# Performance work log

Measured on AMD Instinct MI355X. Metric: run time of the kernel, lower is better.

The kernel has to match this reference:

```python
import jax, jax.numpy as jnp
import numpy as np

D_MODEL = 2048
NUM_Q_HEADS = 16
NUM_KV_HEADS = 4
HEAD_DIM = D_MODEL // NUM_Q_HEADS  # 128
NUM_GROUPS = NUM_Q_HEADS // NUM_KV_HEADS  # 4
ROPE_BASE = 10000.0


def _rope_cos_sin(seq_len, head_dim):
    inv_freq = 1.0 / (ROPE_BASE ** (jnp.arange(0, head_dim, 2, dtype=jnp.float32) / head_dim))
    t = jnp.arange(seq_len, dtype=jnp.float32)
    freqs = jnp.outer(t, inv_freq)            # [S, head_dim/2]
    emb = jnp.concatenate([freqs, freqs], -1)  # [S, head_dim]
    return jnp.cos(emb)[None, :, None, :], jnp.sin(emb)[None, :, None, :]


def _rotate_half(x):
    half = x.shape[-1] // 2
    return jnp.concatenate([-x[..., half:], x[..., :half]], axis=-1)


def setup_inputs() -> dict:
    key = jax.random.key(0)
    k0, k1, k2, k3, k4 = jax.random.split(key, 5)
    B, S = 2, 2048
    kv_dim = HEAD_DIM * NUM_KV_HEADS
    scale = D_MODEL ** -0.5
    return {
        "x": jax.random.normal(k0, (B, S, D_MODEL), jnp.float32),
        "attention_mask": jnp.ones((B, S), jnp.int32),
        "Wq": jax.random.normal(k1, (D_MODEL, D_MODEL), jnp.float32) * scale,
        "Wk": jax.random.normal(k2, (D_MODEL, kv_dim), jnp.float32) * scale,
        "Wv": jax.random.normal(k3, (D_MODEL, kv_dim), jnp.float32) * scale,
        "Wo": jax.random.normal(k4, (D_MODEL, D_MODEL), jnp.float32) * scale,
    }


def reference(x, attention_mask, Wq, Wk, Wv, Wo):
    B, S, _ = x.shape
    q = (x @ Wq).reshape(B, S, NUM_Q_HEADS, HEAD_DIM)
    k = (x @ Wk).reshape(B, S, NUM_KV_HEADS, HEAD_DIM)
    v = (x @ Wv).reshape(B, S, NUM_KV_HEADS, HEAD_DIM)

    cos, sin = _rope_cos_sin(S, HEAD_DIM)  # [1,S,1,hd]
    q = q * cos + _rotate_half(q) * sin
    k = k * cos + _rotate_half(k) * sin

    # [B, H, S, hd]; replicate KV heads across groups (repeat_interleave)
    q = q.transpose(0, 2, 1, 3)
    k = jnp.repeat(k.transpose(0, 2, 1, 3), NUM_GROUPS, axis=1)
    v = jnp.repeat(v.transpose(0, 2, 1, 3), NUM_GROUPS, axis=1)

    scale = HEAD_DIM ** -0.5
    scores = jnp.einsum("bhqd,bhkd->bhqk", q, k) * scale
    mask = attention_mask[:, None, None, :]  # [B,1,1,S] over keys
    scores = jnp.where(mask == 0, jnp.float32(-jnp.inf), scores)
    probs = jax.nn.softmax(scores, axis=-1)
    out = jnp.einsum("bhqk,bhkd->bhqd", probs, v)
    out = out.transpose(0, 2, 1, 3).reshape(B, S, D_MODEL)
    return out @ Wo
```

## Files before the change

kernel.cpp:

```cpp
#include <hip/hip_runtime.h>
#include <hip/hip_bf16.h>

typedef __attribute__((ext_vector_type(4))) float f32x4;
typedef __attribute__((ext_vector_type(16))) float f32x16;
typedef __attribute__((ext_vector_type(8))) short s16x8;
typedef __attribute__((ext_vector_type(4))) short s16x4;
typedef __attribute__((ext_vector_type(2))) unsigned int u32x2;

__device__ __forceinline__ float fexp2(float x) {
    float y; asm("v_exp_f32 %0, %1" : "=v"(y) : "v"(x)); return y;
}

__global__ void rope_tables(float* __restrict__ cosT, float* __restrict__ sinT) {
    const int s = blockIdx.x, j = threadIdx.x;
    const float inv = exp2f(-(float)j * (13.287712379549449f / 64.f));
    const float f = (float)s * inv;
    cosT[s * 64 + j] = cosf(f);
    sinT[s * 64 + j] = sinf(f);
}

__global__ void mask_bias(const int* __restrict__ mask, float* __restrict__ mb, int n) {
    const int i = blockIdx.x * 256 + threadIdx.x;
    if (i < n) mb[i] = (mask[i] == 0) ? -1e30f : 0.f;
}

__global__ __launch_bounds__(256)
void cast_f32_bf16(const float* __restrict__ src, __hip_bfloat16* __restrict__ dst, int n4) {
    const int i = blockIdx.x * 256 + threadIdx.x;
    if (i < n4) {
        f32x4 v = *reinterpret_cast<const f32x4*>(src + (size_t)i * 4);
        union { s16x4 v4; __hip_bfloat16 h[4]; } u;
#pragma unroll
        for (int j = 0; j < 4; ++j) u.h[j] = __float2bfloat16(v[j]);
        *reinterpret_cast<s16x4*>(dst + (size_t)i * 4) = u.v4;
    }
}

__global__ __launch_bounds__(256)
void transpose_cast_all(const float* __restrict__ Wq, const float* __restrict__ Wk,
                        const float* __restrict__ Wv, const float* __restrict__ Wo,
                        __hip_bfloat16* __restrict__ wqkv_t, __hip_bfloat16* __restrict__ wo_t) {
    __shared__ __align__(16) float t[32][33];
    const int tx = threadIdx.x, ty = threadIdx.y;
    const int xseg = blockIdx.x;
    const int r0 = blockIdx.y * 32;
    const float* src; __hip_bfloat16* dst; int C, c0;
    if (xseg < 64)      { src = Wq; dst = wqkv_t;                  C = 2048; c0 = xseg * 32; }
    else if (xseg < 80) { src = Wk; dst = wqkv_t + 2048ULL * 2048; C = 512;  c0 = (xseg - 64) * 32; }
    else if (xseg < 96) { src = Wv; dst = wqkv_t + 2560ULL * 2048; C = 512;  c0 = (xseg - 80) * 32; }
    else                { src = Wo; dst = wo_t;                    C = 2048; c0 = (xseg - 96) * 32; }
#pragma unroll
    for (int i = 0; i < 32; i += 8)
        t[ty + i][tx] = src[(size_t)(r0 + ty + i) * C + c0 + tx];
    __syncthreads();
#pragma unroll
    for (int i = 0; i < 32; i += 8)
        dst[(size_t)(c0 + ty + i) * 2048 + r0 + tx] = __float2bfloat16(t[tx][ty + i]);
}

__global__ __launch_bounds__(256)
void vt_transpose(const __hip_bfloat16* __restrict__ qkv, __hip_bfloat16* __restrict__ Vt) {
    __shared__ unsigned short t[32][33];
    const int tx = threadIdx.x, ty = threadIdx.y;
    const int s0 = blockIdx.x * 32, d0 = blockIdx.y * 32;
    const int bh = blockIdx.z, b = bh >> 2, hh = bh & 3;
    const unsigned short* q = (const unsigned short*)qkv;
#pragma unroll
    for (int i = 0; i < 32; i += 8)
        t[ty + i][tx] = q[(size_t)(b * 2048 + s0 + ty + i) * 3072 + 2560 + hh * 128 + d0 + tx];
    __syncthreads();
#pragma unroll
    for (int i = 0; i < 32; i += 8)
        ((unsigned short*)Vt)[((size_t)(bh * 128) + d0 + ty + i) * 2048 + s0 + tx] = t[tx][ty + i];
}

template<int NI, bool BF16OUT>
__global__ __launch_bounds__(512, 1)
void gemm256_bt(const __hip_bfloat16* __restrict__ A,
                const __hip_bfloat16* __restrict__ Bt,
                void* __restrict__ Cv, int M, int N, int K, int NX) {
    constexpr int NB = NI / 2;
    __shared__ __align__(16) __hip_bfloat16 sm[4][2][8192];
    const int tid = threadIdx.x;
    const int l = tid & 63, w = tid >> 6;
    const int lo = l & 15, hi = l >> 4;
    const int wm = w >> 2, wn = w & 3;
    const int id = blockIdx.x, slot = id >> 3;
    const int by = (id & 7) * 2 + slot / NX;
    const int bx = slot % NX;
    const int row0 = by * 256;
    const int col0 = bx * (NI * 64);
    const int nk = K >> 5;

    f32x4 acc[8][NI];
#pragma unroll
    for (int mi = 0; mi < 8; ++mi)
#pragma unroll
        for (int ni = 0; ni < NI; ++ni) acc[mi][ni] = f32x4{0.f, 0.f, 0.f, 0.f};

    auto stage = [&](int kt) {
        const int s = kt & 3, k0 = kt << 5;
#pragma unroll
        for (int i = 0; i < 2; ++i) {
            const int c = i * 512 + tid;
            const int r = c >> 2, sw = ((c & 3) ^ ((r >> 1) & 3)) * 8;
            __builtin_amdgcn_global_load_lds(
                (const __attribute__((address_space(1))) void*)(A + (size_t)(row0 + r) * K + k0 + sw),
                (__attribute__((address_space(3))) void*)(&sm[s][0][c * 8]), 16, 0, 0);
        }
#pragma unroll
        for (int i = 0; i < NB; ++i) {
            const int c = i * 512 + tid;
            const int r = c >> 2, sw = ((c & 3) ^ ((r >> 1) & 3)) * 8;
            __builtin_amdgcn_global_load_lds(
                (const __attribute__((address_space(1))) void*)(Bt + (size_t)(col0 + r) * K + k0 + sw),
                (__attribute__((address_space(3))) void*)(&sm[s][1][c * 8]), 16, 0, 0);
        }
    };

    stage(0); stage(1); stage(2);
    for (int kt = 0; kt < nk; ++kt) {
        const int s = kt & 3;
        if (kt < nk - 2) {
            if constexpr (NI == 4) asm volatile("s_waitcnt vmcnt(8)" ::: "memory");
            else                   asm volatile("s_waitcnt vmcnt(6)" ::: "memory");
        } else if (kt == nk - 2) {
            if constexpr (NI == 4) asm volatile("s_waitcnt vmcnt(4)" ::: "memory");
            else                   asm volatile("s_waitcnt vmcnt(3)" ::: "memory");
        } else {
            asm volatile("s_waitcnt vmcnt(0)" ::: "memory");
        }
        asm volatile("s_waitcnt lgkmcnt(0)" ::: "memory");
        asm volatile("s_barrier" ::: "memory");
        if (kt + 3 < nk) stage(kt + 3);

        s16x8 af[8], bf[NI];
        const int rsw = ((lo >> 1) & 3);
#pragma unroll
        for (int mi = 0; mi < 8; ++mi)
            af[mi] = *reinterpret_cast<const s16x8*>(
                &sm[s][0][(wm * 128 + mi * 16 + lo) * 32 + ((hi ^ rsw) * 8)]);
#pragma unroll
        for (int ni = 0; ni < NI; ++ni)
            bf[ni] = *reinterpret_cast<const s16x8*>(
                &sm[s][1][(wn * NI * 16 + ni * 16 + lo) * 32 + ((hi ^ rsw) * 8)]);
        __builtin_amdgcn_s_setprio(1);
#pragma unroll
        for (int mi = 0; mi < 8; ++mi)
#pragma unroll
            for (int ni = 0; ni < NI; ++ni)
                acc[mi][ni] = __builtin_amdgcn_mfma_f32_16x16x32_bf16(af[mi], bf[ni], acc[mi][ni], 0, 0, 0);
        __builtin_amdgcn_s_setprio(0);
    }
    const int rbase = row0 + wm * 128 + hi * 4;
    const int cbase = col0 + wn * NI * 16 + lo;
    if constexpr (BF16OUT) {
        __hip_bfloat16* C = (__hip_bfloat16*)Cv;
#pragma unroll
        for (int mi = 0; mi < 8; ++mi)
#pragma unroll
            for (int ni = 0; ni < NI; ++ni)
#pragma unroll
                for (int r = 0; r < 4; ++r)
                    C[(size_t)(rbase + mi * 16 + r) * N + cbase + ni * 16] =
                        __float2bfloat16(acc[mi][ni][r]);
    } else {
        float* C = (float*)Cv;
#pragma unroll
        for (int mi = 0; mi < 8; ++mi)
#pragma unroll
            for (int ni = 0; ni < NI; ++ni)
#pragma unroll
                for (int r = 0; r < 4; ++r)
                    C[(size_t)(rbase + mi * 16 + r) * N + cbase + ni * 16] = acc[mi][ni][r];
    }
}

__global__ __launch_bounds__(256)
void rope_scatter(const __hip_bfloat16* __restrict__ qkv,
                  const float* __restrict__ cosT, const float* __restrict__ sinT,
                  __hip_bfloat16* __restrict__ Qr, __hip_bfloat16* __restrict__ Kr) {
    const int m = blockIdx.y;
    const int col4 = blockIdx.x * 256 + threadIdx.x;
    if (col4 >= 640) return;
    const int col = col4 * 4;
    const int b = m >> 11, s = m & 2047;
    const int d = col & 127;
    const int j = d & 63;
    union { s16x4 v4; __hip_bfloat16 h[4]; } vv, pp, u;
    vv.v4 = *reinterpret_cast<const s16x4*>(qkv + (size_t)m * 3072 + col);
    pp.v4 = *reinterpret_cast<const s16x4*>(qkv + (size_t)m * 3072 + (col ^ 64));
    const f32x4 c4 = *reinterpret_cast<const f32x4*>(cosT + s * 64 + j);
    const f32x4 s4 = *reinterpret_cast<const f32x4*>(sinT + s * 64 + j);
    const float sgn = (d < 64) ? -1.f : 1.f;
#pragma unroll
    for (int i = 0; i < 4; ++i)
        u.h[i] = __float2bfloat16(__bfloat162float(vv.h[i]) * c4[i] +
                                  sgn * __bfloat162float(pp.h[i]) * s4[i]);
    if (col < 2048) {
        const int hh = col >> 7;
        *reinterpret_cast<s16x4*>(&Qr[((size_t)(b * 16 + hh) * 2048 + s) * 128 + d]) = u.v4;
    } else {
        const int hh = (col - 2048) >> 7;
        *reinterpret_cast<s16x4*>(&Kr[((size_t)(b * 4 + hh) * 2048 + s) * 128 + d]) = u.v4;
    }
}

__global__ __launch_bounds__(256, 2)
void attn_kernel(const __hip_bfloat16* __restrict__ Qr,
                 const __hip_bfloat16* __restrict__ Kr,
                 const __hip_bfloat16* __restrict__ Vt,
                 const float* __restrict__ maskb,
                 __hip_bfloat16* __restrict__ Oo) {
    const int S = 2048;
    const int id = blockIdx.x;
    const int v = (id & 7) * 64 + (id >> 3);
    const int qt = v & 15;
    const int bh = v >> 4;
    const int b = bh >> 4, h = bh & 15, kvh = h >> 2;
    const int tid = threadIdx.x;
    const int l = tid & 63, wv_ = tid >> 6;
    const int lq = l & 31, hi2 = l >> 5;
    __shared__ __align__(16) __hip_bfloat16 Ks[2][64 * 128];
    __shared__ __align__(16) __hip_bfloat16 Vs[2][128 * 64];

    const __hip_bfloat16* Qb = Qr + (size_t)(b * 16 + h) * S * 128;
    const __hip_bfloat16* Kb = Kr + (size_t)(b * 4 + kvh) * S * 128;
    const __hip_bfloat16* Vb = Vt + (size_t)(b * 4 + kvh) * 128 * S;
    const float* mrow = maskb + b * S;

    const int qrow = qt * 128 + wv_ * 32 + lq;
    s16x8 qf[8];
#pragma unroll
    for (int ks = 0; ks < 8; ++ks)
        qf[ks] = *reinterpret_cast<const s16x8*>(Qb + (size_t)qrow * 128 + ks * 16 + hi2 * 8);

    float m_run = 0.f, l_run = 0.f;
    f32x16 o[4];
#pragma unroll
    for (int dt = 0; dt < 4; ++dt)
#pragma unroll
        for (int r = 0; r < 16; ++r) o[dt][r] = 0.f;
    const float scale2 = 0.12751682f;

    const int krow = tid >> 4, kc8 = tid & 15;
    const int koff = (kc8 ^ (krow & 7)) * 8;
    const int vrow = tid >> 3, vc8 = tid & 7;
    const int voff = (vc8 ^ (vrow & 7)) * 8;

    s16x8 kreg[4], vreg[4];
    auto load_tile = [&](int kv0) {
#pragma unroll
        for (int i = 0; i < 4; ++i)
            kreg[i] = *reinterpret_cast<const s16x8*>(
                Kb + (size_t)(kv0 + i * 16 + krow) * 128 + kc8 * 8);
#pragma unroll
        for (int i = 0; i < 4; ++i)
            vreg[i] = *reinterpret_cast<const s16x8*>(
                Vb + (size_t)(i * 32 + vrow) * S + kv0 + vc8 * 8);
    };

    auto body = [&](int kt, __hip_bfloat16* Kc, __hip_bfloat16* Vc) {
        const int kv0 = kt * 64;
        f32x4 bi[2][4];
#pragma unroll
        for (int sub = 0; sub < 2; ++sub)
#pragma unroll
            for (int r4 = 0; r4 < 4; ++r4)
                bi[sub][r4] = *reinterpret_cast<const f32x4*>(
                    mrow + kv0 + sub * 32 + r4 * 8 + hi2 * 4);
#pragma unroll
        for (int i = 0; i < 4; ++i)
            *reinterpret_cast<s16x8*>(Kc + (i * 16 + krow) * 128 + koff) = kreg[i];
#pragma unroll
        for (int i = 0; i < 4; ++i)
            *reinterpret_cast<s16x8*>(Vc + (i * 32 + vrow) * 64 + voff) = vreg[i];
        if (kt < 31) load_tile(kv0 + 64);
        asm volatile("s_waitcnt lgkmcnt(0)" ::: "memory");
        asm volatile("s_barrier" ::: "memory");

        f32x16 sc[2];
#pragma unroll
        for (int sub = 0; sub < 2; ++sub)
#pragma unroll
            for (int r = 0; r < 16; ++r) sc[sub][r] = 0.f;
        __builtin_amdgcn_s_setprio(1);
#pragma unroll
        for (int sub = 0; sub < 2; ++sub) {
            const int kr = sub * 32 + lq;
            const int ksw = kr & 7;
#pragma unroll
            for (int ks = 0; ks < 8; ++ks) {
                s16x8 kf = *reinterpret_cast<const s16x8*>(
                    Kc + kr * 128 + (((ks * 2 + hi2) ^ ksw) * 8));
                sc[sub] = __builtin_amdgcn_mfma_f32_32x32x16_bf16(kf, qf[ks], sc[sub], 0, 0, 0);
            }
        }
        __builtin_amdgcn_s_setprio(0);
#pragma unroll
        for (int sub = 0; sub < 2; ++sub)
#pragma unroll
            for (int r = 0; r < 16; ++r)
                sc[sub][r] = fmaf(sc[sub][r], scale2, bi[sub][r >> 2][r & 3]);
        float mx = sc[0][0];
#pragma unroll
        for (int sub = 0; sub < 2; ++sub)
#pragma unroll
            for (int r = 0; r < 16; ++r) mx = fmaxf(mx, sc[sub][r]);
        float ss = 0.f;
#pragma unroll
        for (int sub = 0; sub < 2; ++sub)
#pragma unroll
            for (int r = 0; r < 16; ++r) {
                sc[sub][r] = fexp2(sc[sub][r] - m_run);
                ss += sc[sub][r];
            }
        mx = fmaxf(mx, __shfl_xor(mx, 32));
        if (__ballot(mx > m_run + 11.5417f) != 0ull) {
            const float mnew = fmaxf(m_run, mx);
            const float alpha = fexp2(m_run - mnew);
            m_run = mnew;
            l_run *= alpha;
            ss *= alpha;
#pragma unroll
            for (int sub = 0; sub < 2; ++sub)
#pragma unroll
                for (int r = 0; r < 16; ++r) sc[sub][r] *= alpha;
#pragma unroll
            for (int dt = 0; dt < 4; ++dt)
#pragma unroll
                for (int r = 0; r < 16; ++r) o[dt][r] *= alpha;
        }
        ss += __shfl_xor(ss, 32);
        l_run += ss;
        unsigned int wvp[8][2];
#pragma unroll
        for (int g = 0; g < 8; ++g) {
            const int sub = g >> 2, r4 = g & 3;
            asm("v_cvt_pk_bf16_f32 %0, %1, %2"
                : "=v"(wvp[g][0]) : "v"(sc[sub][r4 * 4 + 0]), "v"(sc[sub][r4 * 4 + 1]));
            asm("v_cvt_pk_bf16_f32 %0, %1, %2"
                : "=v"(wvp[g][1]) : "v"(sc[sub][r4 * 4 + 2]), "v"(sc[sub][r4 * 4 + 3]));
        }
        __builtin_amdgcn_s_setprio(1);
#pragma unroll
        for (int ks = 0; ks < 4; ++ks) {
            u32x2 r0 = __builtin_amdgcn_permlane32_swap(wvp[2 * ks][0], wvp[2 * ks + 1][0], false, false);
            u32x2 r1 = __builtin_amdgcn_permlane32_swap(wvp[2 * ks][1], wvp[2 * ks + 1][1], false, false);
            union { unsigned int u[4]; s16x8 v; } pf;
            pf.u[0] = r0.x; pf.u[1] = r1.x; pf.u[2] = r0.y; pf.u[3] = r1.y;
#pragma unroll
            for (int dt = 0; dt < 4; ++dt) {
                const int dvr = dt * 32 + lq;
                s16x8 vf = *reinterpret_cast<const s16x8*>(
                    Vc + dvr * 64 + (((ks * 2 + hi2) ^ (dvr & 7)) * 8));
                o[dt] = __builtin_amdgcn_mfma_f32_32x32x16_bf16(vf, pf.v, o[dt], 0, 0, 0);
            }
        }
        __builtin_amdgcn_s_setprio(0);
    };

    load_tile(0);
    for (int kt2 = 0; kt2 < 16; ++kt2) {
        body(2 * kt2,     &Ks[0][0], &Vs[0][0]);
        body(2 * kt2 + 1, &Ks[1][0], &Vs[1][0]);
    }
    const float inv = 1.f / l_run;
    const size_t obase = (size_t)(b * S + qt * 128 + wv_ * 32 + lq) * 2048 + h * 128;
#pragma unroll
    for (int dt = 0; dt < 4; ++dt)
#pragma unroll
        for (int r4 = 0; r4 < 4; ++r4) {
            union { s16x4 v4; __hip_bfloat16 hh[4]; } u;
#pragma unroll
            for (int j = 0; j < 4; ++j)
                u.hh[j] = __float2bfloat16(o[dt][r4 * 4 + j] * inv);
            *reinterpret_cast<s16x4*>(&Oo[obase + dt * 32 + r4 * 8 + hi2 * 4]) = u.v4;
        }
}

extern "C" void kernel_launch(void* const* d_in, const int* in_sizes, int n_in,
                              void* d_out, int out_size, void* d_ws, size_t ws_size,
                              hipStream_t stream) {
    const float* x  = (const float*)d_in[0];
    const int* mask = (const int*)d_in[1];
    const float* Wq = (const float*)d_in[2];
    const float* Wk = (const float*)d_in[3];
    const float* Wv = (const float*)d_in[4];
    const float* Wo = (const float*)d_in[5];
    float* out = (float*)d_out;

    char* ws = (char*)d_ws;
    size_t off = 0;
    auto alloc = [&](size_t bytes) -> void* {
        void* p = ws + off;
        off += (bytes + 255) & ~(size_t)255;
        return p;
    };
    __hip_bfloat16* xb     = (__hip_bfloat16*)alloc(4096ULL * 2048 * 2);
    __hip_bfloat16* wqkv_t = (__hip_bfloat16*)alloc(3072ULL * 2048 * 2);
    __hip_bfloat16* wo_t   = (__hip_bfloat16*)alloc(2048ULL * 2048 * 2);
    __hip_bfloat16* qkvb   = (__hip_bfloat16*)alloc(4096ULL * 3072 * 2);
    __hip_bfloat16* Kr     = (__hip_bfloat16*)alloc(2ULL * 4 * 2048 * 128 * 2);
    __hip_bfloat16* Vt     = (__hip_bfloat16*)alloc(2ULL * 4 * 2048 * 128 * 2);
    float*          cosT   = (float*)alloc(2048ULL * 64 * 4);
    float*          sinT   = (float*)alloc(2048ULL * 64 * 4);
    float*          maskb  = (float*)alloc(2ULL * 2048 * 4);
    __hip_bfloat16* attno  = (__hip_bfloat16*)alloc(4096ULL * 2048 * 2);
    __hip_bfloat16* Qr    = xb;

    rope_tables<<<dim3(2048), dim3(64), 0, stream>>>(cosT, sinT);
    mask_bias<<<dim3(16), dim3(256), 0, stream>>>(mask, maskb, 4096);
    cast_f32_bf16<<<dim3(8192), dim3(256), 0, stream>>>(x, xb, 2097152);
    transpose_cast_all<<<dim3(160, 64), dim3(32, 8), 0, stream>>>(Wq, Wk, Wv, Wo, wqkv_t, wo_t);

    gemm256_bt<4, true><<<dim3(192), dim3(512), 0, stream>>>(xb, wqkv_t, qkvb, 4096, 3072, 2048, 12);
    rope_scatter<<<dim3(3, 4096), dim3(256), 0, stream>>>(qkvb, cosT, sinT, Qr, Kr);
    vt_transpose<<<dim3(64, 4, 8), dim3(32, 8), 0, stream>>>(qkvb, Vt);
    attn_kernel<<<dim3(512), dim3(256), 0, stream>>>(Qr, Kr, Vt, maskb, attno);
    gemm256_bt<2, false><<<dim3(256), dim3(512), 0, stream>>>(attno, wo_t, out, 4096, 2048, 2048, 16);
}
```

Baseline: 221.7 us.

## Process two 32-row query sub-tiles per wave in attention kernel

Each wave now handles 64 query rows as two 32-row sub-tiles, so the query tile per block grows from 128 to 256 rows and the grid halves to 256 blocks. Every K and V fragment read from shared memory now feeds two MFMAs, halving LDS traffic and global K/V tile loads per query row. In exchange register pressure roughly doubles (launch bounds drop to one block per SIMD set), occupancy falls, and only 256 blocks cover the 256 CUs, leaving little latency hiding or load balancing.

```diff
diff --git a/kernel.cpp b/kernel.cpp
--- a/kernel.cpp
+++ b/kernel.cpp
@@ -206,7 +206,7 @@
     }
 }
 
-__global__ __launch_bounds__(256, 2)
+__global__ __launch_bounds__(256, 1)
 void attn_kernel(const __hip_bfloat16* __restrict__ Qr,
                  const __hip_bfloat16* __restrict__ Kr,
                  const __hip_bfloat16* __restrict__ Vt,
@@ -214,9 +214,9 @@
                  __hip_bfloat16* __restrict__ Oo) {
     const int S = 2048;
     const int id = blockIdx.x;
-    const int v = (id & 7) * 64 + (id >> 3);
-    const int qt = v & 15;
-    const int bh = v >> 4;
+    const int v = (id & 7) * 32 + (id >> 3);
+    const int qt = v & 7;
+    const int bh = v >> 3;
     const int b = bh >> 4, h = bh & 15, kvh = h >> 2;
     const int tid = threadIdx.x;
     const int l = tid & 63, wv_ = tid >> 6;
@@ -229,18 +229,23 @@
     const __hip_bfloat16* Vb = Vt + (size_t)(b * 4 + kvh) * 128 * S;
     const float* mrow = maskb + b * S;
 
-    const int qrow = qt * 128 + wv_ * 32 + lq;
-    s16x8 qf[8];
-#pragma unroll
-    for (int ks = 0; ks < 8; ++ks)
-        qf[ks] = *reinterpret_cast<const s16x8*>(Qb + (size_t)qrow * 128 + ks * 16 + hi2 * 8);
-
-    float m_run = 0.f, l_run = 0.f;
-    f32x16 o[4];
-#pragma unroll
-    for (int dt = 0; dt < 4; ++dt)
-#pragma unroll
-        for (int r = 0; r < 16; ++r) o[dt][r] = 0.f;
+    const int qrow0 = qt * 256 + wv_ * 64 + lq;
+    s16x8 qf[2][8];
+#pragma unroll
+    for (int qs = 0; qs < 2; ++qs)
+#pragma unroll
+        for (int ks = 0; ks < 8; ++ks)
+            qf[qs][ks] = *reinterpret_cast<const s16x8*>(
+                Qb + (size_t)(qrow0 + qs * 32) * 128 + ks * 16 + hi2 * 8);
+
+    float m_run[2] = {0.f, 0.f}, l_run[2] = {0.f, 0.f};
+    f32x16 o[2][4];
+#pragma unroll
+    for (int qs = 0; qs < 2; ++qs)
+#pragma unroll
+        for (int dt = 0; dt < 4; ++dt)
+#pragma unroll
+            for (int r = 0; r < 16; ++r) o[qs][dt][r] = 0.f;
     const float scale2 = 0.12751682f;
 
     const int krow = tid >> 4, kc8 = tid & 15;
@@ -279,11 +284,13 @@
         asm volatile("s_waitcnt lgkmcnt(0)" ::: "memory");
         asm volatile("s_barrier" ::: "memory");
 
-        f32x16 sc[2];
-#pragma unroll
-        for (int sub = 0; sub < 2; ++sub)
-#pragma unroll
-            for (int r = 0; r < 16; ++r) sc[sub][r] = 0.f;
+        f32x16 sc[2][2];
+#pragma unroll
+        for (int qs = 0; qs < 2; ++qs)
+#pragma unroll
+            for (int sub = 0; sub < 2; ++sub)
+#pragma unroll
+                for (int r = 0; r < 16; ++r) sc[qs][sub][r] = 0.f;
         __builtin_amdgcn_s_setprio(1);
 #pragma unroll
         for (int sub = 0; sub < 2; ++sub) {
@@ -293,68 +300,80 @@
             for (int ks = 0; ks < 8; ++ks) {
                 s16x8 kf = *reinterpret_cast<const s16x8*>(
                     Kc + kr * 128 + (((ks * 2 + hi2) ^ ksw) * 8));
-                sc[sub] = __builtin_amdgcn_mfma_f32_32x32x16_bf16(kf, qf[ks], sc[sub], 0, 0, 0);
+                sc[0][sub] = __builtin_amdgcn_mfma_f32_32x32x16_bf16(kf, qf[0][ks], sc[0][sub], 0, 0, 0);
+                sc[1][sub] = __builtin_amdgcn_mfma_f32_32x32x16_bf16(kf, qf[1][ks], sc[1][sub], 0, 0, 0);
             }
         }
         __builtin_amdgcn_s_setprio(0);
-#pragma unroll
-        for (int sub = 0; sub < 2; ++sub)
-#pragma unroll
-            for (int r = 0; r < 16; ++r)
-                sc[sub][r] = fmaf(sc[sub][r], scale2, bi[sub][r >> 2][r & 3]);
-        float mx = sc[0][0];
-#pragma unroll
-        for (int sub = 0; sub < 2; ++sub)
-#pragma unroll
-            for (int r = 0; r < 16; ++r) mx = fmaxf(mx, sc[sub][r]);
-        float ss = 0.f;
-#pragma unroll
-        for (int sub = 0; sub < 2; ++sub)
-#pragma unroll
-            for (int r = 0; r < 16; ++r) {
-                sc[sub][r] = fexp2(sc[sub][r] - m_run);
-                ss += sc[sub][r];
-            }
-        mx = fmaxf(mx, __shfl_xor(mx, 32));
-        if (__ballot(mx > m_run + 11.5417f) != 0ull) {
-            const float mnew = fmaxf(m_run, mx);
-            const float alpha = fexp2(m_run - mnew);
-            m_run = mnew;
-            l_run *= alpha;
-            ss *= alpha;
+        unsigned int wvp[2][8][2];
+#pragma unroll
+        for (int qs = 0; qs < 2; ++qs) {
 #pragma unroll
             for (int sub = 0; sub < 2; ++sub)
 #pragma unroll
-                for (int r = 0; r < 16; ++r) sc[sub][r] *= alpha;
-#pragma unroll
-            for (int dt = 0; dt < 4; ++dt)
-#pragma unroll
-                for (int r = 0; r < 16; ++r) o[dt][r] *= alpha;
-        }
-        ss += __shfl_xor(ss, 32);
-        l_run += ss;
-        unsigned int wvp[8][2];
-#pragma unroll
-        for (int g = 0; g < 8; ++g) {
-            const int sub = g >> 2, r4 = g & 3;
-            asm("v_cvt_pk_bf16_f32 %0, %1, %2"
-                : "=v"(wvp[g][0]) : "v"(sc[sub][r4 * 4 + 0]), "v"(sc[sub][r4 * 4 + 1]));
-            asm("v_cvt_pk_bf16_f32 %0, %1, %2"
-                : "=v"(wvp[g][1]) : "v"(sc[sub][r4 * 4 + 2]), "v"(sc[sub][r4 * 4 + 3]));
+                for (int r = 0; r < 16; ++r)
+                    sc[qs][sub][r] = fmaf(sc[qs][sub][r], scale2, bi[sub][r >> 2][r & 3]);
+            float mx = sc[qs][0][0];
+#pragma unroll
+            for (int sub = 0; sub < 2; ++sub)
+#pragma unroll
+                for (int r = 0; r < 16; ++r) mx = fmaxf(mx, sc[qs][sub][r]);
+            float ss = 0.f;
+#pragma unroll
+            for (int sub = 0; sub < 2; ++sub)
+#pragma unroll
+                for (int r = 0; r < 16; ++r) {
+                    sc[qs][sub][r] = fexp2(sc[qs][sub][r] - m_run[qs]);
+                    ss += sc[qs][sub][r];
+                }
+            mx = fmaxf(mx, __shfl_xor(mx, 32));
+            if (__ballot(mx > m_run[qs] + 11.5417f) != 0ull) {
+                const float mnew = fmaxf(m_run[qs], mx);
+                const float alpha = fexp2(m_run[qs] - mnew);
+                m_run[qs] = mnew;
+                l_run[qs] *= alpha;
+                ss *= alpha;
+#pragma unroll
+                for (int sub = 0; sub < 2; ++sub)
+#pragma unroll
+                    for (int r = 0; r < 16; ++r) sc[qs][sub][r] *= alpha;
+#pragma unroll
+                for (int dt = 0; dt < 4; ++dt)
+#pragma unroll
+                    for (int r = 0; r < 16; ++r) o[qs][dt][r] *= alpha;
+            }
+            ss += __shfl_xor(ss, 32);
+            l_run[qs] += ss;
+#pragma unroll
+            for (int g = 0; g < 8; ++g) {
+                const int sub = g >> 2, r4 = g & 3;
+                asm("v_cvt_pk_bf16_f32 %0, %1, %2"
+                    : "=v"(wvp[qs][g][0]) : "v"(sc[qs][sub][r4 * 4 + 0]), "v"(sc[qs][sub][r4 * 4 + 1]));
+                asm("v_cvt_pk_bf16_f32 %0, %1, %2"
+                    : "=v"(wvp[qs][g][1]) : "v"(sc[qs][sub][r4 * 4 + 2]), "v"(sc[qs][sub][r4 * 4 + 3]));
+            }
         }
         __builtin_amdgcn_s_setprio(1);
 #pragma unroll
         for (int ks = 0; ks < 4; ++ks) {
-            u32x2 r0 = __builtin_amdgcn_permlane32_swap(wvp[2 * ks][0], wvp[2 * ks + 1][0], false, false);
-            u32x2 r1 = __builtin_amdgcn_permlane32_swap(wvp[2 * ks][1], wvp[2 * ks + 1][1], false, false);
-            union { unsigned int u[4]; s16x8 v; } pf;
-            pf.u[0] = r0.x; pf.u[1] = r1.x; pf.u[2] = r0.y; pf.u[3] = r1.y;
+            union { unsigned int u[4]; s16x8 v; } pf0, pf1;
+            {
+                u32x2 r0 = __builtin_amdgcn_permlane32_swap(wvp[0][2 * ks][0], wvp[0][2 * ks + 1][0], false, false);
+                u32x2 r1 = __builtin_amdgcn_permlane32_swap(wvp[0][2 * ks][1], wvp[0][2 * ks + 1][1], false, false);
+                pf0.u[0] = r0.x; pf0.u[1] = r1.x; pf0.u[2] = r0.y; pf0.u[3] = r1.y;
+            }
+            {
+                u32x2 r0 = __builtin_amdgcn_permlane32_swap(wvp[1][2 * ks][0], wvp[1][2 * ks + 1][0], false, false);
+                u32x2 r1 = __builtin_amdgcn_permlane32_swap(wvp[1][2 * ks][1], wvp[1][2 * ks + 1][1], false, false);
+                pf1.u[0] = r0.x; pf1.u[1] = r1.x; pf1.u[2] = r0.y; pf1.u[3] = r1.y;
+            }
 #pragma unroll
             for (int dt = 0; dt < 4; ++dt) {
                 const int dvr = dt * 32 + lq;
                 s16x8 vf = *reinterpret_cast<const s16x8*>(
                     Vc + dvr * 64 + (((ks * 2 + hi2) ^ (dvr & 7)) * 8));
-                o[dt] = __builtin_amdgcn_mfma_f32_32x32x16_bf16(vf, pf.v, o[dt], 0, 0, 0);
+                o[0][dt] = __builtin_amdgcn_mfma_f32_32x32x16_bf16(vf, pf0.v, o[0][dt], 0, 0, 0);
+                o[1][dt] = __builtin_amdgcn_mfma_f32_32x32x16_bf16(vf, pf1.v, o[1][dt], 0, 0, 0);
             }
         }
         __builtin_amdgcn_s_setprio(0);
@@ -365,18 +384,21 @@
         body(2 * kt2,     &Ks[0][0], &Vs[0][0]);
         body(2 * kt2 + 1, &Ks[1][0], &Vs[1][0]);
     }
-    const float inv = 1.f / l_run;
-    const size_t obase = (size_t)(b * S + qt * 128 + wv_ * 32 + lq) * 2048 + h * 128;
-#pragma unroll
-    for (int dt = 0; dt < 4; ++dt)
-#pragma unroll
-        for (int r4 = 0; r4 < 4; ++r4) {
-            union { s16x4 v4; __hip_bfloat16 hh[4]; } u;
-#pragma unroll
-            for (int j = 0; j < 4; ++j)
-                u.hh[j] = __float2bfloat16(o[dt][r4 * 4 + j] * inv);
-            *reinterpret_cast<s16x4*>(&Oo[obase + dt * 32 + r4 * 8 + hi2 * 4]) = u.v4;
-        }
+#pragma unroll
+    for (int qs = 0; qs < 2; ++qs) {
+        const float inv = 1.f / l_run[qs];
+        const size_t obase = (size_t)(b * S + qt * 256 + wv_ * 64 + qs * 32 + lq) * 2048 + h * 128;
+#pragma unroll
+        for (int dt = 0; dt < 4; ++dt)
+#pragma unroll
+            for (int r4 = 0; r4 < 4; ++r4) {
+                union { s16x4 v4; __hip_bfloat16 hh[4]; } u;
+#pragma unroll
+                for (int j = 0; j < 4; ++j)
+                    u.hh[j] = __float2bfloat16(o[qs][dt][r4 * 4 + j] * inv);
+                *reinterpret_cast<s16x4*>(&Oo[obase + dt * 32 + r4 * 8 + hi2 * 4]) = u.v4;
+            }
+    }
 }
 
 extern "C" void kernel_launch(void* const* d_in, const int* in_sizes, int n_in,
@@ -417,6 +439,6 @@
     gemm256_bt<4, true><<<dim3(192), dim3(512), 0, stream>>>(xb, wqkv_t, qkvb, 4096, 3072, 2048, 12);
     rope_scatter<<<dim3(3, 4096), dim3(256), 0, stream>>>(qkvb, cosT, sinT, Qr, Kr);
     vt_transpose<<<dim3(64, 4, 8), dim3(32, 8), 0, stream>>>(qkvb, Vt);
-    attn_kernel<<<dim3(512), dim3(256), 0, stream>>>(Qr, Kr, Vt, maskb, attno);
+    attn_kernel<<<dim3(256), dim3(256), 0, stream>>>(Qr, Kr, Vt, maskb, attno);
     gemm256_bt<2, false><<<dim3(256), dim3(512), 0, stream>>>(attno, wo_t, out, 4096, 2048, 2048, 16);
 }
```

After: 240.3 us. 1.08x slower.
